# Performance work log

Hardware: AMD Instinct MI355X
Metric: run time of the kernel (lower is better)

The kernel has to match this reference:

```python
import jax, jax.numpy as jnp
import numpy as np

NUM_CLASSES = 1      # hard-coded in panoptic_inference2
MASK_THR = 1e-3      # cur_masks[:, k] >= 0.001


def _panoptic_single(logits, mask_logits, pad):
    # logits: [Q, C+1], mask_logits: [P, Q], pad: [P] bool (all False here)
    scores = logits.max(axis=-1)                      # cur_scores per query
    labels = jnp.argmax(logits, axis=-1)              # predicted class per query
    keep = labels != NUM_CLASSES                      # drop 'no-object' queries

    m = jax.nn.sigmoid(mask_logits)                   # [P, Q] cur_masks
    prob_masks = scores[None, :] * m                  # cur_prob_masks [P, Q]
    # emulate column selection cur_masks[:, keep] by masking with -inf
    masked = jnp.where(keep[None, :], prob_masks, -jnp.inf)

    # probabilities = softmax over (kept) queries; max_confs = per-point max prob
    soft = jax.nn.softmax(masked, axis=1)             # [P, Q]
    max_confs = soft.max(axis=1)                      # [P]

    # cur_mask_ids = argmax over kept queries (indices in full query space)
    mid = jnp.argmax(masked, axis=1)                  # [P]
    m_sel = jnp.take_along_axis(m, mid[:, None], axis=1)[:, 0]
    # point contributes to segment k iff argmax==k AND sigmoid>=thr (and not padded)
    valid = (m_sel >= MASK_THR) & (~pad) & keep[mid]  # [P]

    Q = logits.shape[0]
    # per-query area of mask = (mid==k) & thr ; segment kept iff nonempty
    counts = jnp.zeros((Q,), jnp.int32).at[mid].add(valid.astype(jnp.int32))
    nonempty = counts > 0
    # sequential segment ids in query order (masks are disjoint, so the
    # conf-based reordering in the original cannot change sem/ins)
    seg_id = jnp.cumsum(nonempty.astype(jnp.int32))   # [Q]

    ins = jnp.where(valid, seg_id[mid], 0).astype(jnp.int32)
    sem = jnp.where(valid, labels[mid].astype(jnp.int32), 0)
    return sem, ins, max_confs


def setup_inputs() -> dict:
    key = jax.random.key(0)
    k1, k2 = jax.random.split(key)
    B, P, Q, C1 = 2, 200000, 100, NUM_CLASSES + 1
    pred_logits = jax.random.normal(k1, (B, Q, C1), dtype=jnp.float32)
    pred_masks = jax.random.normal(k2, (B, P, Q), dtype=jnp.float32)
    padding = jnp.zeros((B, P), dtype=bool)
    return {"pred_logits": pred_logits, "pred_masks": pred_masks, "padding": padding}


def reference(pred_logits, pred_masks, padding):
    sem, ins, max_confs = jax.vmap(_panoptic_single)(pred_logits, pred_masks, padding)
    return sem, ins, max_confs
```

## Files before the change

### kernel.cpp

```cpp
#include <hip/hip_runtime.h>
#include <math.h>

#define B_    2
#define P_    200000
#define Q_    100
#define TPB   5
#define GXB   625
#define TB    25600


__device__ __forceinline__ void dma16(const void* g, void* l) {
    __builtin_amdgcn_global_load_lds(
        (const __attribute__((address_space(1))) void*)g,
        (__attribute__((address_space(3))) void*)l, 16, 0, 0);
}

__global__ __launch_bounds__(256) void pano_pass1(
    const float* __restrict__ logits,
    const float* __restrict__ masks,
    const unsigned char* __restrict__ pad,
    float* __restrict__ out,
    ulonglong2* __restrict__ flags)
{
    const int b = blockIdx.y, tid = threadIdx.x;
    __shared__ __align__(16) float s_tile[2][TB / 4];
    __shared__ float s_msc[Q_];
    __shared__ int   s_flag[Q_];
    if (tid < Q_) {
        float l0 = logits[(b * Q_ + tid) * 2 + 0];
        float l1 = logits[(b * Q_ + tid) * 2 + 1];
        s_msc[tid]  = (l1 > l0) ? -1e30f : fmaxf(l0, l1);
        s_flag[tid] = 0;
    }

    const int wave = tid >> 6, wl = tid & 63, g = wl >> 2, l = wl & 3;
    const char* mb = (const char*)(masks + (size_t)b * P_ * Q_);
    const int t0 = blockIdx.x * TPB;

    auto stage = [&](int t, int buf) {
        const char* gb = mb + (size_t)t * TB;
        char* lb = (char*)&s_tile[buf][0];
        #pragma unroll
        for (int i = 0; i < 7; ++i) {
            int c = wave + 4 * i;
            if (c < 25) dma16(gb + c * 1024 + wl * 16, lb + c * 1024);
        }
    };

    stage(t0, 0);
    int buf = 0;

    for (int ti = 0; ti < TPB; ++ti) {
        __syncthreads();
        if (ti + 1 < TPB) stage(t0 + ti + 1, buf ^ 1);

        const int t = t0 + ti;
        const int r = wave * 16 + g;
        const int p = t * 64 + r;
        const char*  lrow = (const char*)&s_tile[buf][0] + r * 400;
        const float* rowp = (const float*)(mb + (size_t)p * 400);

        float S0 = 0.0f;
        float v1 = -INFINITY, v2 = -INFINITY, m1 = 0.0f;
        int   q1 = -1;

        #pragma unroll
        for (int k = 0; k < 7; ++k) {
            const bool act = (k < 6) || (l == 0);
            const int  qb  = (k < 6) ? (16 * k + 4 * l) : 96;
            float4 v4 = *(const float4*)(lrow + ((k < 6) ? (64 * k + 16 * l) : 384));
            float xv[4] = {v4.x, v4.y, v4.z, v4.w};
            #pragma unroll
            for (int e = 0; e < 4; ++e) {
                int q = qb + e;
                float m   = __builtin_amdgcn_rcpf(1.0f + __expf(-xv[e]));
                float val = act ? s_msc[q] * m : -INFINITY;
                S0 += __expf(val);
                bool tk = val > v1;
                v2 = tk ? v1 : fmaxf(v2, val);
                v1 = tk ? val : v1;
                m1 = tk ? m   : m1;
                q1 = tk ? q   : q1;
            }
        }

        #pragma unroll
        for (int off = 1; off <= 2; off <<= 1) {
            float So  = __shfl_xor(S0, off, 64);
            float v1o = __shfl_xor(v1, off, 64);
            float v2o = __shfl_xor(v2, off, 64);
            float m1o = __shfl_xor(m1, off, 64);
            int   q1o = __shfl_xor(q1, off, 64);
            S0 += So;
            bool tk = (v1o > v1) || (v1o == v1 && (unsigned)q1o < (unsigned)q1);
            v2 = fmaxf(fminf(v1, v1o), fmaxf(v2, v2o));
            v1 = tk ? v1o : v1;
            m1 = tk ? m1o : m1;
            q1 = tk ? q1o : q1;
        }

        if (l == 0 && (v1 - v2) < 5e-5f) {
            float bv = -INFINITY, bm = 0.0f; int bq = -1;
            for (int q = 0; q < Q_; ++q) {
                float x = rowp[q];
                float e = expf(-x);
                float m = 1.0f / (1.0f + e);
                float vv = s_msc[q] * m;
                if (vv > bv) { bv = vv; bq = q; bm = m; }
            }
            q1 = bq; m1 = bm;
        }

        bool valid = (q1 >= 0) && (s_msc[q1] > -1e29f) &&
                     (m1 >= 1e-3f) &&
                     (pad[(size_t)b * P_ + p] == 0);

        float conf = __expf(v1) * __builtin_amdgcn_rcpf(S0);
        float insf = valid ? (float)q1 : -1.0f;
        if (l == 0 && valid) s_flag[q1] = 1;

        int   src    = (wl & 15) * 4;
        float conf_g = __shfl(conf, src, 64);
        float insf_g = __shfl(insf, src, 64);
        if (wl < 16) {
            int prow = t * 64 + wave * 16 + wl;
            size_t o = (size_t)b * P_ + prow;
            out[o]                       = 0.0f;
            out[(size_t)B_ * P_ + o]     = insf_g;
            out[2 * (size_t)B_ * P_ + o] = conf_g;
        }
        buf ^= 1;
    }

    __syncthreads();
    {
        bool f = (tid < Q_) ? (s_flag[tid] != 0) : false;
        unsigned long long m = __ballot(f);
        if (tid == 0)  flags[b * GXB + blockIdx.x].x = m;
        if (tid == 64) flags[b * GXB + blockIdx.x].y = m;
    }
}

__global__ __launch_bounds__(256) void pano_pass2(
    const ulonglong2* __restrict__ flags,
    int* __restrict__ seg)
{
    const int b = blockIdx.x, tid = threadIdx.x;
    unsigned long long m0 = 0ull, m1 = 0ull;
    for (int i = tid; i < GXB; i += 256) {
        ulonglong2 w = flags[b * GXB + i];
        m0 |= w.x; m1 |= w.y;
    }
    #pragma unroll
    for (int off = 32; off; off >>= 1) {
        m0 |= __shfl_xor(m0, off, 64);
        m1 |= __shfl_xor(m1, off, 64);
    }
    __shared__ unsigned long long sm0[4], sm1[4];
    if ((tid & 63) == 0) { sm0[tid >> 6] = m0; sm1[tid >> 6] = m1; }
    __syncthreads();
    if (tid == 0) {
        m0 = sm0[0] | sm0[1] | sm0[2] | sm0[3];
        m1 = sm1[0] | sm1[1] | sm1[2] | sm1[3];
        int c = 0;
        for (int q = 0; q < Q_; ++q) {
            c += (int)((q < 64 ? (m0 >> q) : (m1 >> (q - 64))) & 1ull);
            seg[b * Q_ + q] = c;
        }
    }
}

__global__ __launch_bounds__(256) void pano_pass3(
    const int* __restrict__ seg,
    float* __restrict__ out)
{
    const int b = blockIdx.y, tid = threadIdx.x;
    __shared__ int s_seg[Q_];
    if (tid < Q_) s_seg[tid] = seg[b * Q_ + tid];
    __syncthreads();

    int p = blockIdx.x * blockDim.x + tid;
    if (p < P_) {
        size_t o = (size_t)B_ * P_ + (size_t)b * P_ + p;
        float f = out[o];
        out[o] = (f >= 0.0f) ? (float)s_seg[(int)f] : 0.0f;
    }
}

extern "C" void kernel_launch(void* const* d_in, const int* in_sizes, int n_in,
                              void* d_out, int out_size, void* d_ws, size_t ws_size,
                              hipStream_t stream) {
    const float* logits = (const float*)d_in[0];
    const float* masks  = (const float*)d_in[1];
    const unsigned char* pad = (const unsigned char*)d_in[2];
    float* out = (float*)d_out;

    ulonglong2* flags = (ulonglong2*)d_ws;
    int*        seg   = (int*)((char*)d_ws + 20480);

    dim3 block(256);
    pano_pass1<<<dim3(GXB, B_), block, 0, stream>>>(logits, masks, pad, out, flags);
    pano_pass2<<<dim3(B_), block, 0, stream>>>(flags, seg);
    pano_pass3<<<dim3((P_ + 255) / 256, B_), block, 0, stream>>>(seg, out);
}
```

Baseline: 251.2 us.

## Replace LDS DMA staging with register double-buffered direct loads in grid-stride loop

Drops the global_load_lds shared-memory double buffer and has each thread load its row slice straight into registers with nontemporal float4 loads, prefetching the next tile into a second register set while processing the current one. The grid becomes a persistent grid-stride loop of 1024 blocks per batch over 3125 tiles, with the flags workspace resized to match. This cuts LDS traffic and occupancy pressure but uses uncoalesced per-thread 400-byte row strides and more registers. Tiles are no longer split evenly across blocks, so some blocks do one more tile than others.

```diff
diff --git a/kernel.cpp b/kernel.cpp
--- a/kernel.cpp
+++ b/kernel.cpp
@@ -1,19 +1,14 @@
 #include <hip/hip_runtime.h>
 #include <math.h>
 
-#define B_    2
-#define P_    200000
-#define Q_    100
-#define TPB   5
-#define GXB   625
-#define TB    25600
-
-
-__device__ __forceinline__ void dma16(const void* g, void* l) {
-    __builtin_amdgcn_global_load_lds(
-        (const __attribute__((address_space(1))) void*)g,
-        (__attribute__((address_space(3))) void*)l, 16, 0, 0);
-}
+#define B_   2
+#define P_   200000
+#define Q_   100
+#define NIT  3125
+#define GX   1024
+
+typedef float f4 __attribute__((ext_vector_type(4)));
+
 
 __global__ __launch_bounds__(256) void pano_pass1(
     const float* __restrict__ logits,
@@ -23,7 +18,6 @@
     ulonglong2* __restrict__ flags)
 {
     const int b = blockIdx.y, tid = threadIdx.x;
-    __shared__ __align__(16) float s_tile[2][TB / 4];
     __shared__ float s_msc[Q_];
     __shared__ int   s_flag[Q_];
     if (tid < Q_) {
@@ -32,33 +26,24 @@
         s_msc[tid]  = (l1 > l0) ? -1e30f : fmaxf(l0, l1);
         s_flag[tid] = 0;
     }
-
-    const int wave = tid >> 6, wl = tid & 63, g = wl >> 2, l = wl & 3;
-    const char* mb = (const char*)(masks + (size_t)b * P_ * Q_);
-    const int t0 = blockIdx.x * TPB;
-
-    auto stage = [&](int t, int buf) {
-        const char* gb = mb + (size_t)t * TB;
-        char* lb = (char*)&s_tile[buf][0];
+    __syncthreads();
+
+    const int wave = tid >> 6, wl = tid & 63;
+    const int g = wl >> 2, l = wl & 3;
+    const int rbase = wave * 16 + g;
+    const float* mb = masks + (size_t)b * P_ * Q_;
+
+    auto loadrow = [&](f4* v, int t) {
+        const f4* grow = (const f4*)(mb + ((size_t)t * 64 + rbase) * Q_);
         #pragma unroll
-        for (int i = 0; i < 7; ++i) {
-            int c = wave + 4 * i;
-            if (c < 25) dma16(gb + c * 1024 + wl * 16, lb + c * 1024);
-        }
+        for (int k = 0; k < 6; ++k)
+            v[k] = __builtin_nontemporal_load(grow + (k * 4 + l));
+        v[6] = __builtin_nontemporal_load(grow + 24);
     };
 
-    stage(t0, 0);
-    int buf = 0;
-
-    for (int ti = 0; ti < TPB; ++ti) {
-        __syncthreads();
-        if (ti + 1 < TPB) stage(t0 + ti + 1, buf ^ 1);
-
-        const int t = t0 + ti;
-        const int r = wave * 16 + g;
-        const int p = t * 64 + r;
-        const char*  lrow = (const char*)&s_tile[buf][0] + r * 400;
-        const float* rowp = (const float*)(mb + (size_t)p * 400);
+    auto process = [&](int t, const f4* v) {
+        const int p = t * 64 + rbase;
+        const float* rowp = mb + (size_t)p * Q_;
 
         float S0 = 0.0f;
         float v1 = -INFINITY, v2 = -INFINITY, m1 = 0.0f;
@@ -68,8 +53,7 @@
         for (int k = 0; k < 7; ++k) {
             const bool act = (k < 6) || (l == 0);
             const int  qb  = (k < 6) ? (16 * k + 4 * l) : 96;
-            float4 v4 = *(const float4*)(lrow + ((k < 6) ? (64 * k + 16 * l) : 384));
-            float xv[4] = {v4.x, v4.y, v4.z, v4.w};
+            float xv[4] = {v[k].x, v[k].y, v[k].z, v[k].w};
             #pragma unroll
             for (int e = 0; e < 4; ++e) {
                 int q = qb + e;
@@ -129,15 +113,31 @@
             out[(size_t)B_ * P_ + o]     = insf_g;
             out[2 * (size_t)B_ * P_ + o] = conf_g;
         }
-        buf ^= 1;
+    };
+
+    f4 va[7], vb[7];
+    int it = blockIdx.x;
+    loadrow(va, it);
+    while (true) {
+        int itn = min(it + GX, NIT - 1);
+        loadrow(vb, itn);
+        process(it, va);
+        if (it + GX >= NIT) break;
+        it = itn;
+
+        int itn2 = min(it + GX, NIT - 1);
+        loadrow(va, itn2);
+        process(it, vb);
+        if (it + GX >= NIT) break;
+        it = itn2;
     }
 
     __syncthreads();
     {
         bool f = (tid < Q_) ? (s_flag[tid] != 0) : false;
         unsigned long long m = __ballot(f);
-        if (tid == 0)  flags[b * GXB + blockIdx.x].x = m;
-        if (tid == 64) flags[b * GXB + blockIdx.x].y = m;
+        if (tid == 0)  flags[b * GX + blockIdx.x].x = m;
+        if (tid == 64) flags[b * GX + blockIdx.x].y = m;
     }
 }
 
@@ -147,8 +147,8 @@
 {
     const int b = blockIdx.x, tid = threadIdx.x;
     unsigned long long m0 = 0ull, m1 = 0ull;
-    for (int i = tid; i < GXB; i += 256) {
-        ulonglong2 w = flags[b * GXB + i];
+    for (int i = tid; i < GX; i += 256) {
+        ulonglong2 w = flags[b * GX + i];
         m0 |= w.x; m1 |= w.y;
     }
     #pragma unroll
@@ -196,10 +196,10 @@
     float* out = (float*)d_out;
 
     ulonglong2* flags = (ulonglong2*)d_ws;
-    int*        seg   = (int*)((char*)d_ws + 20480);
+    int*        seg   = (int*)((char*)d_ws + 40960);
 
     dim3 block(256);
-    pano_pass1<<<dim3(GXB, B_), block, 0, stream>>>(logits, masks, pad, out, flags);
+    pano_pass1<<<dim3(GX, B_), block, 0, stream>>>(logits, masks, pad, out, flags);
     pano_pass2<<<dim3(B_), block, 0, stream>>>(flags, seg);
     pano_pass3<<<dim3((P_ + 255) / 256, B_), block, 0, stream>>>(seg, out);
 }
```

After: 253.7 us. About the same (+1.0%).
